# Optimization experiments

Measured on AMD Instinct MI355X. Metric: run time of the kernel, lower is better.

The kernel has to match this reference:

```python
import jax, jax.numpy as jnp
import numpy as np

G = 4          # n_groups
KG = 1         # kernel_groups[stage]
KS = 8         # kernel_sizes[stage]
EIN = 64       # eff_in_dim = in_dim // n_groups
EOUT = 64      # eff_out_dim
PIN = 32       # in_points
POUT = 128     # out_points
QD = 256       # query_dim
EPS = 1e-5


def _ln(x, axes):
    m = jnp.mean(x, axis=axes, keepdims=True)
    v = jnp.var(x, axis=axes, keepdims=True)
    return (x - m) * jax.lax.rsqrt(v + EPS)


def setup_inputs() -> dict:
    key = jax.random.key(0)
    ks = jax.random.split(key, 14)
    B, N = 8, 300
    s = 0.02
    common_out = G * (EIN * EOUT + PIN * POUT)  # 32768
    priv_out = 2 * G * KG * KS * KS             # 512
    flat = EOUT * POUT * G                      # 32768
    return {
        "stage": 0,
        "x": jax.random.normal(ks[0], (B, N, G, PIN, EIN), jnp.float32),
        "query": jax.random.normal(ks[1], (B, N, QD), jnp.float32),
        "cpg_w": jax.random.normal(ks[2], (common_out, QD), jnp.float32) * s,
        "cpg_b": jax.random.normal(ks[3], (common_out,), jnp.float32) * s,
        "ppg_w": jax.random.normal(ks[4], (priv_out, QD), jnp.float32) * s,
        "ppg_b": jax.random.normal(ks[5], (priv_out,), jnp.float32) * s,
        "ml": jax.random.normal(ks[6], (G * KG, EIN, KS), jnp.float32) * 0.1,
        "mr": jax.random.normal(ks[7], (G * KG, KS, EOUT), jnp.float32) * 0.1,
        "sl": jax.random.normal(ks[8], (G * KG, POUT, KS), jnp.float32) * 0.1,
        "sr": jax.random.normal(ks[9], (G * KG, KS, PIN), jnp.float32) * 0.1,
        "base_w": jax.random.normal(ks[10], (QD, flat), jnp.float32) * s,
        "lora_A": jax.random.normal(ks[11], (64, flat), jnp.float32) * s,
        "lora_B": jax.random.normal(ks[12], (QD, 64), jnp.float32) * s,
        "out_bias": jnp.zeros((QD,), jnp.float32),
        "gamma": jnp.ones((QD,), jnp.float32),
        "beta": jnp.zeros((QD,), jnp.float32),
    }


def reference(stage, x, query, cpg_w, cpg_b, ppg_w, ppg_b, ml, mr, sl, sr,
              base_w, lora_A, lora_B, out_bias, gamma, beta):
    B, N, g, P, C = x.shape
    BN = B * N
    q = query.reshape(BN, QD)

    # common (query-generated) mixing params
    common = (q @ cpg_w.T + cpg_b).reshape(BN, G, EIN * EOUT + PIN * POUT)
    Mc = common[..., : EIN * EOUT].reshape(BN, G, EIN, EOUT)
    Sc = common[..., EIN * EOUT :].reshape(BN, G, POUT, PIN)

    # private factorized params: ml @ mz @ mr, sl @ sz @ sr
    priv = (q @ ppg_w.T + ppg_b).reshape(BN, 2, G * KG, KS, KS)
    mz, sz = priv[:, 0], priv[:, 1]
    Mp = jnp.einsum("gik,bgkl,glj->bgij", ml, mz, mr)  # (BN, G*KG, EIN, EOUT)
    Sp = jnp.einsum("gik,bgkl,glj->bgij", sl, sz, sr)  # (BN, G*KG, POUT, PIN)

    M = Mc + Mp.reshape(BN, G, KG, EIN, EOUT).sum(axis=2)
    S = Sc + Sp.reshape(BN, G, KG, POUT, PIN).sum(axis=2)

    out = x.reshape(BN, G, P, C)
    # adaptive channel mixing + LN over last two dims + ReLU
    out = jnp.einsum("bgpc,bgcd->bgpd", out, M)
    out = jax.nn.relu(_ln(out, (-2, -1)))
    # adaptive spatial mixing + LN + ReLU
    out = jnp.einsum("bgop,bgpd->bgod", S, out)  # (BN, G, POUT, EOUT)
    out = jax.nn.relu(_ln(out, (-2, -1)))

    # low-rank-adjusted linear projection to query dim
    out = out.reshape(B, N, G * POUT * EOUT)
    W = base_w + lora_B @ lora_A  # (QD, flat)
    out = out @ W.T + out_bias

    # residual + affine LayerNorm
    y = query + out
    return _ln(y, (-1,)) * gamma + beta
```

## Files before the change

### kernel.cpp

```cpp
#include <hip/hip_runtime.h>
#include <hip/hip_bf16.h>

#define BN_TOK 2400
#define QDIM   256
#define NG     4
#define FLAT   32768
#define GSZ    8192
#define KSP    16
#define LN_EPS 1e-5f
#define PPAD   42
#define CSLD   136

typedef __attribute__((ext_vector_type(8))) short bf16x8;
typedef __attribute__((ext_vector_type(4))) float f32x4;
typedef __hip_bfloat16 bf16;

__device__ __forceinline__ float bf2f(ushort u) {
  union { unsigned int i; float f; } c;
  c.i = ((unsigned int)u) << 16;
  return c.f;
}
__device__ __forceinline__ ushort f2u(float f) {
  bf16 h = __float2bfloat16(f);
  union { bf16 h; ushort u; } c; c.h = h; return c.u;
}

__device__ __forceinline__ int xcdswz(int orig, int nwg) {
  int xcd = orig & 7, base = orig >> 3;
  int q = nwg >> 3, r = nwg & 7;
  int start = (xcd < r) ? xcd * (q + 1) : r * (q + 1) + (xcd - r) * q;
  return start + base;
}

__global__ __launch_bounds__(256) void cast_k(const float* __restrict__ in,
                                              bf16* __restrict__ out, int n4) {
  int i = blockIdx.x * 256 + threadIdx.x;
  if (i < n4) {
    float4 v = ((const float4*)in)[i];
    bf16 tmp[4] = {__float2bfloat16(v.x), __float2bfloat16(v.y),
                   __float2bfloat16(v.z), __float2bfloat16(v.w)};
    ((ushort4*)out)[i] = *(const ushort4*)tmp;
  }
}

__global__ __launch_bounds__(256) void build_weff_k(
    const float* __restrict__ cpg_w, const float* __restrict__ cpg_b,
    const float* __restrict__ ppg_w, const float* __restrict__ ppg_b,
    const float* __restrict__ ml, const float* __restrict__ mr,
    const float* __restrict__ sl, const float* __restrict__ sr,
    bf16* __restrict__ Weff, float* __restrict__ bias_eff) {
  int tid = threadIdx.x;
  int rb = blockIdx.x;
  int g = blockIdx.y;
  int part = blockIdx.z;
  int pbase = part * 256 + g * 64;

  float pw[64];
#pragma unroll
  for (int kl = 0; kl < 64; ++kl)
    pw[kl] = ppg_w[(size_t)(pbase + kl) * QDIM + tid];

  if (part == 0) {
    int d = rb;
    float t[8];
#pragma unroll
    for (int k = 0; k < 8; ++k) {
      float s = 0.f;
#pragma unroll
      for (int l = 0; l < 8; ++l) s += mr[g * 512 + l * 64 + d] * pw[k * 8 + l];
      t[k] = s;
    }
    for (int r = 0; r < 64; ++r) {
      int outrow = g * GSZ + d * 64 + r;
      int srcrow = g * GSZ + r * 64 + d;
      float acc = cpg_w[(size_t)srcrow * QDIM + tid];
#pragma unroll
      for (int k = 0; k < 8; ++k) acc += ml[g * 512 + r * 8 + k] * t[k];
      Weff[(size_t)outrow * QDIM + tid] = __float2bfloat16(acc);
    }
    if (tid < 64) {
      int r = tid;
      float b = cpg_b[g * GSZ + r * 64 + d];
#pragma unroll
      for (int k = 0; k < 8; ++k) {
        float s = 0.f;
#pragma unroll
        for (int l = 0; l < 8; ++l)
          s += mr[g * 512 + l * 64 + d] * ppg_b[pbase + k * 8 + l];
        b += ml[g * 512 + r * 8 + k] * s;
      }
      bias_eff[g * GSZ + d * 64 + r] = b;
    }
  } else {
    int o0 = rb * 2;
    float t0v[8], t1v[8];
#pragma unroll
    for (int l = 0; l < 8; ++l) {
      float s0 = 0.f, s1 = 0.f;
#pragma unroll
      for (int k = 0; k < 8; ++k) {
        s0 += sl[g * 1024 + o0 * 8 + k] * pw[k * 8 + l];
        s1 += sl[g * 1024 + (o0 + 1) * 8 + k] * pw[k * 8 + l];
      }
      t0v[l] = s0; t1v[l] = s1;
    }
    for (int r = 0; r < 32; ++r) {
      int rr = rb * 64 + r;
      int p = rr & 31;
      int row = g * GSZ + 4096 + rr;
      float acc = cpg_w[(size_t)row * QDIM + tid];
#pragma unroll
      for (int l = 0; l < 8; ++l) acc += sr[g * 256 + l * 32 + p] * t0v[l];
      Weff[(size_t)row * QDIM + tid] = __float2bfloat16(acc);
    }
    for (int r = 32; r < 64; ++r) {
      int rr = rb * 64 + r;
      int p = rr & 31;
      int row = g * GSZ + 4096 + rr;
      float acc = cpg_w[(size_t)row * QDIM + tid];
#pragma unroll
      for (int l = 0; l < 8; ++l) acc += sr[g * 256 + l * 32 + p] * t1v[l];
      Weff[(size_t)row * QDIM + tid] = __float2bfloat16(acc);
    }
    if (tid < 64) {
      int rr = rb * 64 + tid;
      int o = rr >> 5, p = rr & 31;
      int row = g * GSZ + 4096 + rr;
      float b = cpg_b[row];
#pragma unroll
      for (int l = 0; l < 8; ++l) {
        float s = 0.f;
#pragma unroll
        for (int k = 0; k < 8; ++k)
          s += sl[g * 1024 + o * 8 + k] * ppg_b[pbase + k * 8 + l];
        b += sr[g * 256 + l * 32 + p] * s;
      }
      bias_eff[row] = b;
    }
  }
}

__global__ __launch_bounds__(256) void build_wb_k(
    const float* __restrict__ base_w, const float* __restrict__ lora_A,
    const float* __restrict__ lora_B, bf16* __restrict__ Wb) {
  int jb = blockIdx.x * 256;
  int i0 = blockIdx.y * 16;
  int tid = threadIdx.x;
  __shared__ float lB[16][64];
  for (int e = tid; e < 16 * 64; e += 256)
    lB[e >> 6][e & 63] = lora_B[(size_t)(i0 + (e >> 6)) * 64 + (e & 63)];
  __syncthreads();
  int j = jb + tid;
  float acc[16] = {};
  for (int r = 0; r < 64; ++r) {
    float la = lora_A[(size_t)r * FLAT + j];
#pragma unroll
    for (int i = 0; i < 16; ++i) acc[i] += lB[i][r] * la;
  }
#pragma unroll
  for (int i = 0; i < 16; ++i)
    Wb[(size_t)(i0 + i) * FLAT + j] =
        __float2bfloat16(base_w[(size_t)(i0 + i) * FLAT + j] + acc[i]);
}

template <bool OBF>
__global__ __launch_bounds__(256) void gemm_nt(
    const bf16* __restrict__ A, const bf16* __restrict__ B,
    const float* __restrict__ bias, void* __restrict__ Cout,
    int M, int lda, int ldb, int Kslice, int ldc) {
  __shared__ __align__(16) ushort smem[128 * CSLD];
  ushort* As = smem;
  ushort* Bs = smem + 8192;
  int tid = threadIdx.x;
  int w = tid >> 6, lane = tid & 63;
  int nwg = gridDim.x * gridDim.y;
  int swz = xcdswz(blockIdx.x + gridDim.x * blockIdx.y, nwg);
  int m0 = (swz % gridDim.x) * 128, n0 = (swz / gridDim.x) * 128;
  int kbase = blockIdx.z * Kslice;
  int wm = (w & 1) * 64, wn = (w >> 1) * 64;
  f32x4 acc[4][4] = {};
  for (int kb = 0; kb < Kslice; kb += 64) {
#pragma unroll
    for (int i = 0; i < 4; ++i) {
      int c = (i * 4 + w) * 64 + lane;
      int row = c >> 3, slot = c & 7;
      int ss = slot ^ (row & 7);
      int grow = m0 + row; if (grow >= M) grow = M - 1;
      const bf16* src = A + (size_t)grow * lda + kbase + kb + ss * 8;
      __builtin_amdgcn_global_load_lds(
          (const __attribute__((address_space(1))) void*)src,
          (__attribute__((address_space(3))) void*)(As + (size_t)c * 8), 16, 0, 0);
    }
#pragma unroll
    for (int i = 0; i < 4; ++i) {
      int c = (i * 4 + w) * 64 + lane;
      int row = c >> 3, slot = c & 7;
      int ss = slot ^ (row & 7);
      const bf16* src = B + (size_t)(n0 + row) * ldb + kbase + kb + ss * 8;
      __builtin_amdgcn_global_load_lds(
          (const __attribute__((address_space(1))) void*)src,
          (__attribute__((address_space(3))) void*)(Bs + (size_t)c * 8), 16, 0, 0);
    }
    __syncthreads();
#pragma unroll
    for (int ks = 0; ks < 2; ++ks) {
      int sl = ks * 4 + (lane >> 4);
      bf16x8 af[4], bfr[4];
#pragma unroll
      for (int i = 0; i < 4; ++i) {
        int r = wm + i * 16 + (lane & 15);
        af[i] = *(const bf16x8*)&As[r * 64 + (sl ^ (r & 7)) * 8];
        int cc = wn + i * 16 + (lane & 15);
        bfr[i] = *(const bf16x8*)&Bs[cc * 64 + (sl ^ (cc & 7)) * 8];
      }
#pragma unroll
      for (int i = 0; i < 4; ++i)
#pragma unroll
        for (int j = 0; j < 4; ++j)
          acc[i][j] = __builtin_amdgcn_mfma_f32_16x16x32_bf16(bfr[j], af[i], acc[i][j], 0, 0, 0);
    }
    __syncthreads();
  }
  if constexpr (OBF) {
#pragma unroll
    for (int i = 0; i < 4; ++i) {
      int ml_ = wm + i * 16 + (lane & 15);
#pragma unroll
      for (int j = 0; j < 4; ++j) {
        int nl = wn + j * 16 + (lane >> 4) * 4;
        float4 b4 = bias ? *(const float4*)&bias[n0 + nl] : make_float4(0.f, 0.f, 0.f, 0.f);
        ushort4 uv = {f2u(acc[i][j][0] + b4.x), f2u(acc[i][j][1] + b4.y),
                      f2u(acc[i][j][2] + b4.z), f2u(acc[i][j][3] + b4.w)};
        *(ushort4*)&smem[ml_ * CSLD + nl] = uv;
      }
    }
    __syncthreads();
    bf16* co = (bf16*)Cout;
#pragma unroll
    for (int it = 0; it < 4; ++it) {
      int row = it * 32 + (tid >> 3);
      int sub = (tid & 7) * 8;
      int gm = m0 + row;
      if (gm < M) {
        size_t base = ((size_t)blockIdx.z * M + gm) * ldc + n0;
        bf16x8 v0 = *(const bf16x8*)&smem[row * CSLD + sub];
        bf16x8 v1 = *(const bf16x8*)&smem[row * CSLD + 64 + sub];
        *(bf16x8*)(co + base + sub) = v0;
        *(bf16x8*)(co + base + 64 + sub) = v1;
      }
    }
  } else {
#pragma unroll
    for (int i = 0; i < 4; ++i) {
      int m = m0 + wm + i * 16 + (lane & 15);
      if (m >= M) continue;
      size_t ro = (size_t)blockIdx.z * M + m;
#pragma unroll
      for (int j = 0; j < 4; ++j) {
        int nb = n0 + wn + j * 16 + (lane >> 4) * 4;
        float4 b4 = bias ? *(const float4*)&bias[nb] : make_float4(0.f, 0.f, 0.f, 0.f);
        *(float4*)((float*)Cout + ro * ldc + nb) =
            make_float4(acc[i][j][0] + b4.x, acc[i][j][1] + b4.y,
                        acc[i][j][2] + b4.z, acc[i][j][3] + b4.w);
      }
    }
  }
}

__device__ __forceinline__ void block_red2(float& s, float& sq, float* redS,
                                           float* redQ, int tid) {
#pragma unroll
  for (int off = 32; off > 0; off >>= 1) {
    s += __shfl_down(s, off);
    sq += __shfl_down(sq, off);
  }
  int w = tid >> 6;
  if ((tid & 63) == 0) { redS[w] = s; redQ[w] = sq; }
  __syncthreads();
  s = redS[0] + redS[1] + redS[2] + redS[3];
  sq = redQ[0] + redQ[1] + redQ[2] + redQ[3];
}

__global__ __launch_bounds__(256) void chain_k(
    const float* __restrict__ x, bf16* __restrict__ common) {
  int tid = threadIdx.x;
  int tl = blockIdx.x;
  int g = blockIdx.y;
  int lane = tid & 63, w = tid >> 6;

  __shared__ ushort o1Tb[64 * PPAD];
  __shared__ float redS[4], redQ[4];

  bf16* cm = common + (size_t)tl * FLAT + g * GSZ;
  const ushort* cmu = (const ushort*)cm;
  int dlane = w * 16 + (lane & 15);

  const float* xg = x + ((size_t)tl * NG + g) * 2048;
  f32x4 a1[2] = {};
#pragma unroll
  for (int ks = 0; ks < 2; ++ks) {
    bf16x8 af = *(const bf16x8*)&cmu[dlane * 64 + ks * 32 + (lane >> 4) * 8];
#pragma unroll
    for (int pt = 0; pt < 2; ++pt) {
      int p = pt * 16 + (lane & 15);
      int k = ks * 32 + (lane >> 4) * 8;
      const float4* xp = (const float4*)(xg + p * 64 + k);
      float4 f0 = xp[0], f1 = xp[1];
      bf16x8 bx;
      bx[0] = (short)f2u(f0.x); bx[1] = (short)f2u(f0.y);
      bx[2] = (short)f2u(f0.z); bx[3] = (short)f2u(f0.w);
      bx[4] = (short)f2u(f1.x); bx[5] = (short)f2u(f1.y);
      bx[6] = (short)f2u(f1.z); bx[7] = (short)f2u(f1.w);
      a1[pt] = __builtin_amdgcn_mfma_f32_16x16x32_bf16(af, bx, a1[pt], 0, 0, 0);
    }
  }
  {
    float s = 0.f, sq = 0.f;
#pragma unroll
    for (int pt = 0; pt < 2; ++pt)
#pragma unroll
      for (int r = 0; r < 4; ++r) { float v = a1[pt][r]; s += v; sq += v * v; }
    block_red2(s, sq, redS, redQ, tid);
    float mean = s * (1.f / 2048.f);
    float var = sq * (1.f / 2048.f) - mean * mean;
    float rs = rsqrtf(var + LN_EPS);
#pragma unroll
    for (int pt = 0; pt < 2; ++pt)
#pragma unroll
      for (int r = 0; r < 4; ++r) {
        float v = (a1[pt][r] - mean) * rs;
        if (v < 0.f) v = 0.f;
        int d = w * 16 + (lane >> 4) * 4 + r;
        int p = pt * 16 + (lane & 15);
        o1Tb[d * PPAD + p] = f2u(v);
      }
  }
  __syncthreads();

  f32x4 a2[2][4] = {};
  {
    bf16x8 bfd[4];
#pragma unroll
    for (int dj = 0; dj < 4; ++dj)
      bfd[dj] = *(const bf16x8*)&o1Tb[(dj * 16 + (lane & 15)) * PPAD + (lane >> 4) * 8];
#pragma unroll
    for (int oi = 0; oi < 2; ++oi) {
      int o = (2 * w + oi) * 16 + (lane & 15);
      bf16x8 sf = *(const bf16x8*)&cmu[4096 + o * 32 + (lane >> 4) * 8];
#pragma unroll
      for (int dj = 0; dj < 4; ++dj)
        a2[oi][dj] = __builtin_amdgcn_mfma_f32_16x16x32_bf16(bfd[dj], sf, a2[oi][dj], 0, 0, 0);
    }
  }
  {
    float s = 0.f, sq = 0.f;
#pragma unroll
    for (int oi = 0; oi < 2; ++oi)
#pragma unroll
      for (int dj = 0; dj < 4; ++dj)
#pragma unroll
        for (int r = 0; r < 4; ++r) { float v = a2[oi][dj][r]; s += v; sq += v * v; }
    block_red2(s, sq, redS, redQ, tid);
    float mean = s * (1.f / 8192.f);
    float var = sq * (1.f / 8192.f) - mean * mean;
    float rs = rsqrtf(var + LN_EPS);
    ushort* cw = (ushort*)cm;
#pragma unroll
    for (int oi = 0; oi < 2; ++oi) {
      int o = (2 * w + oi) * 16 + (lane & 15);
#pragma unroll
      for (int dj = 0; dj < 4; ++dj) {
        int d0 = dj * 16 + (lane >> 4) * 4;
        ushort4 uv;
#pragma unroll
        for (int r = 0; r < 4; ++r) {
          float v = (a2[oi][dj][r] - mean) * rs;
          if (v < 0.f) v = 0.f;
          ((ushort*)&uv)[r] = f2u(v);
        }
        *(ushort4*)&cw[o * 64 + d0] = uv;
      }
    }
  }
}

__global__ __launch_bounds__(256) void finish_k(
    const float* __restrict__ partial, const float* __restrict__ query,
    const float* __restrict__ out_bias, const float* __restrict__ gamma,
    const float* __restrict__ beta, float* __restrict__ out, int t0, int M) {
  int tid = threadIdx.x;
  int tl = blockIdx.x;
  int t = t0 + tl;
  __shared__ float redS[4], redQ[4];
  float s = 0.f;
  for (int ks = 0; ks < KSP; ++ks)
    s += partial[((size_t)ks * M + tl) * QDIM + tid];
  float v = s + out_bias[tid] + query[(size_t)t * QDIM + tid];
  float sum = v, sqv = v * v;
  block_red2(sum, sqv, redS, redQ, tid);
  float mean = sum * (1.f / 256.f);
  float var = sqv * (1.f / 256.f) - mean * mean;
  out[(size_t)t * QDIM + tid] =
      (v - mean) * rsqrtf(var + LN_EPS) * gamma[tid] + beta[tid];
}

extern "C" void kernel_launch(void* const* d_in, const int* in_sizes, int n_in,
                              void* d_out, int out_size, void* d_ws, size_t ws_size,
                              hipStream_t stream) {
  const float* x       = (const float*)d_in[1];
  const float* query   = (const float*)d_in[2];
  const float* cpg_w   = (const float*)d_in[3];
  const float* cpg_b   = (const float*)d_in[4];
  const float* ppg_w   = (const float*)d_in[5];
  const float* ppg_b   = (const float*)d_in[6];
  const float* ml      = (const float*)d_in[7];
  const float* mr      = (const float*)d_in[8];
  const float* sl      = (const float*)d_in[9];
  const float* sr      = (const float*)d_in[10];
  const float* base_w  = (const float*)d_in[11];
  const float* lora_A  = (const float*)d_in[12];
  const float* lora_B  = (const float*)d_in[13];
  const float* out_bias= (const float*)d_in[14];
  const float* gamma   = (const float*)d_in[15];
  const float* beta    = (const float*)d_in[16];
  float* out = (float*)d_out;

  float* wsf = (float*)d_ws;
  bf16*  Wb      = (bf16*)(wsf + 0);
  bf16*  Weff    = (bf16*)(wsf + 4194304);
  float* bias_eff= wsf + 8388608;
  bf16*  qb      = (bf16*)(wsf + 8421376);
  size_t fixedF  = 8728576;
  int CT = (ws_size >= (fixedF + (size_t)BN_TOK * 20480) * sizeof(float)) ? BN_TOK : 600;
  int NCH = BN_TOK / CT;
  bf16*  commonb = (bf16*)(wsf + fixedF);
  float* partialb= wsf + fixedF + (size_t)CT * 16384;

  build_weff_k<<<dim3(64, NG, 2), 256, 0, stream>>>(
      cpg_w, cpg_b, ppg_w, ppg_b, ml, mr, sl, sr, Weff, bias_eff);
  cast_k<<<dim3(BN_TOK * QDIM / 4 / 256), 256, 0, stream>>>(query, qb, BN_TOK * QDIM / 4);
  build_wb_k<<<dim3(FLAT / 256, QDIM / 16), 256, 0, stream>>>(base_w, lora_A, lora_B, Wb);

  for (int ch = 0; ch < NCH; ++ch) {
    int t0 = ch * CT;
    gemm_nt<true><<<dim3((CT + 127) / 128, FLAT / 128, 1), 256, 0, stream>>>(
        qb + (size_t)t0 * QDIM, Weff, bias_eff, commonb, CT, QDIM, QDIM, QDIM, FLAT);
    chain_k<<<dim3(CT, NG), 256, 0, stream>>>(x + (size_t)t0 * GSZ, commonb);
    gemm_nt<false><<<dim3((CT + 127) / 128, QDIM / 128, KSP), 256, 0, stream>>>(
        commonb, Wb, nullptr, partialb, CT, FLAT, FLAT, FLAT / KSP, QDIM);
    finish_k<<<dim3(CT), 256, 0, stream>>>(partialb, query, out_bias, gamma, beta, out, t0, CT);
  }
}
```

Measured before the change: 311.7 us.

## Double-buffer GEMM K-loop and stage chain kernel operands through LDS

The GEMM now keeps two LDS buffers and issues the global-to-LDS loads for the next K tile before the MFMA work on the current one, so copies overlap compute and one barrier per iteration goes away. The bf16 epilogue store is reorganised so each thread writes a single 16-byte chunk per row. The chain kernel first loads M, S and x into padded LDS tiles with coalesced vector loads, converting x to bf16 only once. It also stages the output in LDS before writing it back with coalesced stores. The cost is double the GEMM shared memory, which may lower occupancy, plus extra LDS traffic and barriers in the chain kernel.

New measurement: 313.6 us. No clear change (+0.6%).

```diff
diff --git a/kernel.cpp b/kernel.cpp
--- a/kernel.cpp
+++ b/kernel.cpp
@@ -168,9 +168,7 @@
     const bf16* __restrict__ A, const bf16* __restrict__ B,
     const float* __restrict__ bias, void* __restrict__ Cout,
     int M, int lda, int ldb, int Kslice, int ldc) {
-  __shared__ __align__(16) ushort smem[128 * CSLD];
-  ushort* As = smem;
-  ushort* Bs = smem + 8192;
+  __shared__ __align__(16) ushort smem[32768];
   int tid = threadIdx.x;
   int w = tid >> 6, lane = tid & 63;
   int nwg = gridDim.x * gridDim.y;
@@ -178,30 +176,34 @@
   int m0 = (swz % gridDim.x) * 128, n0 = (swz / gridDim.x) * 128;
   int kbase = blockIdx.z * Kslice;
   int wm = (w & 1) * 64, wn = (w >> 1) * 64;
-  f32x4 acc[4][4] = {};
-  for (int kb = 0; kb < Kslice; kb += 64) {
+
+  auto stage = [&](int buf, int kk) {
 #pragma unroll
     for (int i = 0; i < 4; ++i) {
       int c = (i * 4 + w) * 64 + lane;
       int row = c >> 3, slot = c & 7;
       int ss = slot ^ (row & 7);
       int grow = m0 + row; if (grow >= M) grow = M - 1;
-      const bf16* src = A + (size_t)grow * lda + kbase + kb + ss * 8;
+      const bf16* srcA = A + (size_t)grow * lda + kk + ss * 8;
       __builtin_amdgcn_global_load_lds(
-          (const __attribute__((address_space(1))) void*)src,
-          (__attribute__((address_space(3))) void*)(As + (size_t)c * 8), 16, 0, 0);
-    }
-#pragma unroll
-    for (int i = 0; i < 4; ++i) {
-      int c = (i * 4 + w) * 64 + lane;
-      int row = c >> 3, slot = c & 7;
-      int ss = slot ^ (row & 7);
-      const bf16* src = B + (size_t)(n0 + row) * ldb + kbase + kb + ss * 8;
+          (const __attribute__((address_space(1))) void*)srcA,
+          (__attribute__((address_space(3))) void*)(smem + buf * 16384 + (size_t)c * 8), 16, 0, 0);
+      const bf16* srcB = B + (size_t)(n0 + row) * ldb + kk + ss * 8;
       __builtin_amdgcn_global_load_lds(
-          (const __attribute__((address_space(1))) void*)src,
-          (__attribute__((address_space(3))) void*)(Bs + (size_t)c * 8), 16, 0, 0);
-    }
-    __syncthreads();
+          (const __attribute__((address_space(1))) void*)srcB,
+          (__attribute__((address_space(3))) void*)(smem + buf * 16384 + 8192 + (size_t)c * 8), 16, 0, 0);
+    }
+  };
+
+  f32x4 acc[4][4] = {};
+  int nt = Kslice >> 6;
+  stage(0, kbase);
+  __syncthreads();
+  int cur = 0;
+  for (int t = 0; t < nt; ++t) {
+    if (t + 1 < nt) stage(cur ^ 1, kbase + (t + 1) * 64);
+    const ushort* As = smem + cur * 16384;
+    const ushort* Bs = As + 8192;
 #pragma unroll
     for (int ks = 0; ks < 2; ++ks) {
       int sl = ks * 4 + (lane >> 4);
@@ -220,7 +222,9 @@
           acc[i][j] = __builtin_amdgcn_mfma_f32_16x16x32_bf16(bfr[j], af[i], acc[i][j], 0, 0, 0);
     }
     __syncthreads();
-  }
+    cur ^= 1;
+  }
+
   if constexpr (OBF) {
 #pragma unroll
     for (int i = 0; i < 4; ++i) {
@@ -237,16 +241,13 @@
     __syncthreads();
     bf16* co = (bf16*)Cout;
 #pragma unroll
-    for (int it = 0; it < 4; ++it) {
-      int row = it * 32 + (tid >> 3);
-      int sub = (tid & 7) * 8;
+    for (int it = 0; it < 8; ++it) {
+      int row = it * 16 + (tid >> 4);
+      int sub = (tid & 15) * 8;
       int gm = m0 + row;
       if (gm < M) {
-        size_t base = ((size_t)blockIdx.z * M + gm) * ldc + n0;
-        bf16x8 v0 = *(const bf16x8*)&smem[row * CSLD + sub];
-        bf16x8 v1 = *(const bf16x8*)&smem[row * CSLD + 64 + sub];
-        *(bf16x8*)(co + base + sub) = v0;
-        *(bf16x8*)(co + base + 64 + sub) = v1;
+        *(bf16x8*)(co + ((size_t)blockIdx.z * M + gm) * ldc + n0 + sub) =
+            *(const bf16x8*)&smem[row * CSLD + sub];
       }
     }
   } else {
@@ -288,29 +289,48 @@
   int g = blockIdx.y;
   int lane = tid & 63, w = tid >> 6;
 
-  __shared__ ushort o1Tb[64 * PPAD];
+  __shared__ __align__(16) ushort sm[14720];
   __shared__ float redS[4], redQ[4];
+  ushort* Mt = sm;
+  ushort* Ss = sm + 4608;
+  ushort* xbs = sm + 9728;
+  ushort* o1Tb = sm + 12032;
 
   bf16* cm = common + (size_t)tl * FLAT + g * GSZ;
   const ushort* cmu = (const ushort*)cm;
+  const float* xg = x + ((size_t)tl * NG + g) * 2048;
+
+#pragma unroll
+  for (int it = 0; it < 2; ++it) {
+    int idx = it * 256 + tid;
+    int e = idx * 8;
+    {
+      bf16x8 v = *(const bf16x8*)&cmu[e];
+      *(bf16x8*)&Mt[(e >> 6) * 72 + (e & 63)] = v;
+    }
+    {
+      bf16x8 v = *(const bf16x8*)&cmu[4096 + e];
+      *(bf16x8*)&Ss[(e >> 5) * 40 + (e & 31)] = v;
+    }
+    {
+      int fi = it * 256 + tid;
+      float4 v = ((const float4*)xg)[fi];
+      int fl = fi * 4;
+      ushort4 u = {f2u(v.x), f2u(v.y), f2u(v.z), f2u(v.w)};
+      *(ushort4*)&xbs[(fl >> 6) * 72 + (fl & 63)] = u;
+    }
+  }
+  __syncthreads();
+
   int dlane = w * 16 + (lane & 15);
-
-  const float* xg = x + ((size_t)tl * NG + g) * 2048;
   f32x4 a1[2] = {};
 #pragma unroll
   for (int ks = 0; ks < 2; ++ks) {
-    bf16x8 af = *(const bf16x8*)&cmu[dlane * 64 + ks * 32 + (lane >> 4) * 8];
+    bf16x8 af = *(const bf16x8*)&Mt[dlane * 72 + ks * 32 + (lane >> 4) * 8];
 #pragma unroll
     for (int pt = 0; pt < 2; ++pt) {
       int p = pt * 16 + (lane & 15);
-      int k = ks * 32 + (lane >> 4) * 8;
-      const float4* xp = (const float4*)(xg + p * 64 + k);
-      float4 f0 = xp[0], f1 = xp[1];
-      bf16x8 bx;
-      bx[0] = (short)f2u(f0.x); bx[1] = (short)f2u(f0.y);
-      bx[2] = (short)f2u(f0.z); bx[3] = (short)f2u(f0.w);
-      bx[4] = (short)f2u(f1.x); bx[5] = (short)f2u(f1.y);
-      bx[6] = (short)f2u(f1.z); bx[7] = (short)f2u(f1.w);
+      bf16x8 bx = *(const bf16x8*)&xbs[p * 72 + ks * 32 + (lane >> 4) * 8];
       a1[pt] = __builtin_amdgcn_mfma_f32_16x16x32_bf16(af, bx, a1[pt], 0, 0, 0);
     }
   }
@@ -346,7 +366,7 @@
 #pragma unroll
     for (int oi = 0; oi < 2; ++oi) {
       int o = (2 * w + oi) * 16 + (lane & 15);
-      bf16x8 sf = *(const bf16x8*)&cmu[4096 + o * 32 + (lane >> 4) * 8];
+      bf16x8 sf = *(const bf16x8*)&Ss[o * 40 + (lane >> 4) * 8];
 #pragma unroll
       for (int dj = 0; dj < 4; ++dj)
         a2[oi][dj] = __builtin_amdgcn_mfma_f32_16x16x32_bf16(bfd[dj], sf, a2[oi][dj], 0, 0, 0);
@@ -364,7 +384,6 @@
     float mean = s * (1.f / 8192.f);
     float var = sq * (1.f / 8192.f) - mean * mean;
     float rs = rsqrtf(var + LN_EPS);
-    ushort* cw = (ushort*)cm;
 #pragma unroll
     for (int oi = 0; oi < 2; ++oi) {
       int o = (2 * w + oi) * 16 + (lane & 15);
@@ -378,8 +397,17 @@
           if (v < 0.f) v = 0.f;
           ((ushort*)&uv)[r] = f2u(v);
         }
-        *(ushort4*)&cw[o * 64 + d0] = uv;
-      }
+        *(ushort4*)&sm[o * 72 + d0] = uv;
+      }
+    }
+  }
+  __syncthreads();
+  {
+    ushort* cw = (ushort*)cm;
+#pragma unroll
+    for (int it = 0; it < 4; ++it) {
+      int e = (it * 256 + tid) * 8;
+      *(bf16x8*)&cw[e] = *(const bf16x8*)&sm[(e >> 6) * 72 + (e & 63)];
     }
   }
 }
```
